# Performance work log

Measured on AMD Instinct MI355X. Metric: run time of the kernel, lower is better.

The kernel has to match this reference:

```python
import jax, jax.numpy as jnp
import numpy as np

# module hyperparameters (init kwargs)
D_MODEL = 1024
NUM_HEADS = 16
D_K = D_MODEL // NUM_HEADS
WINDOW_SIZE = 256
GLOBAL_TOKENS = 64
SEQ_LEN = 4096
BATCH = 1
NEG_INF = float('-inf')


def build_local_window_mask(seq_len, window_size, global_tokens):
    # 0 where attention is allowed, -inf where blocked
    i = jnp.arange(seq_len)[:, None]
    j = jnp.arange(seq_len)[None, :]
    allowed = (i < global_tokens) | (j < global_tokens) | (jnp.abs(i - j) <= window_size)
    return jnp.where(allowed, 0.0, NEG_INF).astype(jnp.float32)


def setup_inputs() -> dict:
    key = jax.random.key(0)
    ks = jax.random.split(key, 12)
    s = 1.0 / np.sqrt(D_MODEL)
    inp = {
        'q': jax.random.normal(ks[0], (BATCH, SEQ_LEN, D_MODEL), jnp.float32),
        'k': jax.random.normal(ks[1], (BATCH, SEQ_LEN, D_MODEL), jnp.float32),
        'v': jax.random.normal(ks[2], (BATCH, SEQ_LEN, D_MODEL), jnp.float32),
        # nn.Linear weights: shape (out, in), applied as x @ W.T + b
        'w_q': jax.random.normal(ks[3], (D_MODEL, D_MODEL), jnp.float32) * s,
        'b_q': jax.random.normal(ks[4], (D_MODEL,), jnp.float32) * s,
        'w_k': jax.random.normal(ks[5], (D_MODEL, D_MODEL), jnp.float32) * s,
        'b_k': jax.random.normal(ks[6], (D_MODEL,), jnp.float32) * s,
        'w_v': jax.random.normal(ks[7], (D_MODEL, D_MODEL), jnp.float32) * s,
        'b_v': jax.random.normal(ks[8], (D_MODEL,), jnp.float32) * s,
        'w_o': jax.random.normal(ks[9], (D_MODEL, D_MODEL), jnp.float32) * s,
        'b_o': jax.random.normal(ks[10], (D_MODEL,), jnp.float32) * s,
    }
    return inp


def reference(q, k, v, w_q, b_q, w_k, b_k, w_v, b_v, w_o, b_o):
    B, S, _ = q.shape
    scale = 1.0 / np.sqrt(D_K)

    def proj(x, w, b):  # (B,S,D) -> (B,H,S,Dk)
        y = x @ w.T + b
        return y.reshape(B, S, NUM_HEADS, D_K).transpose(0, 2, 1, 3)

    Q = proj(q, w_q, b_q)
    K = proj(k, w_k, b_k)
    V = proj(v, w_v, b_v)

    local_mask = build_local_window_mask(S, WINDOW_SIZE, GLOBAL_TOKENS)  # (S,S)
    scores = jnp.einsum('bhqd,bhkd->bhqk', Q, K) * scale + local_mask[None, None]
    attn = jax.nn.softmax(scores, axis=-1)
    out = jnp.einsum('bhqk,bhkd->bhqd', attn, V)  # (B,H,S,Dk)
    out = out.transpose(0, 2, 1, 3).reshape(B, S, D_MODEL)
    return out @ w_o.T + b_o
```

## Files before the change

kernel.cpp:

```cpp
#include <hip/hip_runtime.h>

#define S_LEN 4096
#define DMODEL 1024
#define NHEADS 16
#define DKH 64
#define WIN 256
#define GTOK 64
#define NSPLIT 8

typedef unsigned short u16t;
typedef __attribute__((ext_vector_type(8))) short short8;
typedef __attribute__((ext_vector_type(4))) float f32x4;

__device__ __forceinline__ u16t f2bf(float x) {
  union { float f; unsigned int u; } v; v.f = x;
  unsigned int r = v.u + 0x7FFFu + ((v.u >> 16) & 1u);
  return (u16t)(r >> 16);
}

__device__ __forceinline__ void gload_lds16(const u16t* g, u16t* l) {
  __builtin_amdgcn_global_load_lds(
      (const __attribute__((address_space(1))) void*)g,
      (__attribute__((address_space(3))) void*)l, 16, 0, 0);
}

__global__ void cvt4_kernel(const float* __restrict__ s0, const float* __restrict__ s1,
                            const float* __restrict__ s2, const float* __restrict__ s3,
                            u16t* __restrict__ d0, u16t* __restrict__ d1,
                            u16t* __restrict__ d2, u16t* __restrict__ d3) {
  size_t i = (size_t)blockIdx.x * 1024 + threadIdx.x * 4;
  int which = (int)(i >> 20);
  size_t local = i & ((1u << 20) - 1);
  const float* s = which == 0 ? s0 : which == 1 ? s1 : which == 2 ? s2 : s3;
  u16t* d = which == 0 ? d0 : which == 1 ? d1 : which == 2 ? d2 : d3;
  float4 f = *(const float4*)(s + local);
  unsigned int lo = (unsigned int)f2bf(f.x) | ((unsigned int)f2bf(f.y) << 16);
  unsigned int hi = (unsigned int)f2bf(f.z) | ((unsigned int)f2bf(f.w) << 16);
  *(uint2*)(d + local) = make_uint2(lo, hi);
}

__global__ void cvt3_kernel(const float* __restrict__ s0, const float* __restrict__ s1,
                            const float* __restrict__ s2,
                            u16t* __restrict__ d0, u16t* __restrict__ d1,
                            u16t* __restrict__ d2) {
  size_t i = (size_t)blockIdx.x * 1024 + threadIdx.x * 4;
  int which = (int)(i >> 22);
  size_t local = i & ((1u << 22) - 1);
  const float* s = which == 0 ? s0 : which == 1 ? s1 : s2;
  u16t* d = which == 0 ? d0 : which == 1 ? d1 : d2;
  float4 f = *(const float4*)(s + local);
  unsigned int lo = (unsigned int)f2bf(f.x) | ((unsigned int)f2bf(f.y) << 16);
  unsigned int hi = (unsigned int)f2bf(f.z) | ((unsigned int)f2bf(f.w) << 16);
  *(uint2*)(d + local) = make_uint2(lo, hi);
}

#define BN 128
#define GBK 64

template<int OUT_F32, int BMT>
__device__ __forceinline__
void gemm_body(const u16t* __restrict__ A, const u16t* __restrict__ B,
               const float* __restrict__ bias, void* __restrict__ Y,
               int N, int K, float alpha, int m0, int n0)
{
  constexpr int MF = BMT / 32;
  constexpr int CA_ISS = BMT * 2 / 64;

  __shared__ __align__(16) u16t sA[BMT * GBK];
  __shared__ __align__(16) u16t sB[BN * GBK];

  const int tid = threadIdx.x;
  const int lane = tid & 63;
  const int lr = lane & 15, lg = lane >> 4;
  const int w = tid >> 6;
  const int wm = (w >> 1) * (MF * 16), wn = (w & 1) * 64;

  f32x4 acc[MF][4] = {};
  const int nk = K / GBK;

  for (int kt = 0; kt < nk; ++kt) {
    if (kt) __syncthreads();
#pragma unroll
    for (int i = 0; i < CA_ISS; ++i) {
      int c0 = w * (BMT * 2) + i * 64;
      int c = c0 + lane;
      int row = c >> 3, g = (c & 7) ^ (row & 7);
      gload_lds16(A + (size_t)(m0 + row) * K + kt * GBK + g * 8, sA + (size_t)c0 * 8);
    }
#pragma unroll
    for (int i = 0; i < 4; ++i) {
      int c0 = w * 256 + i * 64;
      int c = c0 + lane;
      int row = c >> 3, g = (c & 7) ^ (row & 7);
      gload_lds16(B + (size_t)(n0 + row) * K + kt * GBK + g * 8, sB + (size_t)c0 * 8);
    }
    __syncthreads();

    short8 af[MF][2], bf[4][2];
#pragma unroll
    for (int mf = 0; mf < MF; ++mf)
#pragma unroll
      for (int kk = 0; kk < 2; ++kk) {
        int s = ((kk * 4 + lg) ^ (lr & 7));
        af[mf][kk] = *(const short8*)&sA[(wm + mf * 16 + lr) * GBK + s * 8];
      }
#pragma unroll
    for (int nf = 0; nf < 4; ++nf)
#pragma unroll
      for (int kk = 0; kk < 2; ++kk) {
        int s = ((kk * 4 + lg) ^ (lr & 7));
        bf[nf][kk] = *(const short8*)&sB[(wn + nf * 16 + lr) * GBK + s * 8];
      }
#pragma unroll
    for (int kk = 0; kk < 2; ++kk)
#pragma unroll
      for (int mf = 0; mf < MF; ++mf)
#pragma unroll
        for (int nf = 0; nf < 4; ++nf)
          acc[mf][nf] = __builtin_amdgcn_mfma_f32_16x16x32_bf16(af[mf][kk], bf[nf][kk], acc[mf][nf], 0, 0, 0);
  }

#pragma unroll
  for (int nf = 0; nf < 4; ++nf) {
    int col = n0 + wn + nf * 16 + lr;
    float bv = bias[col];
#pragma unroll
    for (int mf = 0; mf < MF; ++mf)
#pragma unroll
      for (int r = 0; r < 4; ++r) {
        int row = m0 + wm + mf * 16 + lg * 4 + r;
        float v = (acc[mf][nf][r] + bv) * alpha;
        if (OUT_F32) ((float*)Y)[(size_t)row * N + col] = v;
        else         ((u16t*)Y)[(size_t)row * N + col] = f2bf(v);
      }
  }
}

#define QSCALE 0.18033688011112042f
__global__ __launch_bounds__(256)
void gemm_qkv(const u16t* __restrict__ xq, const u16t* __restrict__ xk, const u16t* __restrict__ xv,
              const u16t* __restrict__ wq, const u16t* __restrict__ wk, const u16t* __restrict__ wv,
              const float* __restrict__ bq, const float* __restrict__ bk, const float* __restrict__ bv,
              u16t* __restrict__ Qp, u16t* __restrict__ Kp, u16t* __restrict__ Vp)
{
  int b = blockIdx.x;
  int wid = (b & 7) * 96 + (b >> 3);
  int z = wid >> 8;
  int rem = wid & 255;
  int my = rem >> 3, mx = rem & 7;
  const u16t* A = z == 0 ? xq : z == 1 ? xk : xv;
  const u16t* B = z == 0 ? wq : z == 1 ? wk : wv;
  const float* bi = z == 0 ? bq : z == 1 ? bk : bv;
  u16t* Y = z == 0 ? Qp : z == 1 ? Kp : Vp;
  const float alpha = (z == 0) ? QSCALE : 1.0f;
  gemm_body<0, 128>(A, B, bi, Y, DMODEL, DMODEL, alpha, my * 128, mx * BN);
}

__global__ __launch_bounds__(256)
void gemm_o(const u16t* __restrict__ A, const u16t* __restrict__ B,
            const float* __restrict__ bias, float* __restrict__ Y)
{
  int b = blockIdx.x;
  int wid = (b & 7) * 64 + (b >> 3);
  int my = wid >> 3, mx = wid & 7;
  gemm_body<1, 64>(A, B, bias, Y, DMODEL, DMODEL, 1.0f, my * 64, mx * BN);
}

#define KLDT 72

__global__ __launch_bounds__(256)
void attn_kernel(const u16t* __restrict__ Qp, const u16t* __restrict__ Kp,
                 const u16t* __restrict__ Vp, u16t* __restrict__ AO,
                 float* __restrict__ pacc, float* __restrict__ pml)
{
  __shared__ __align__(16) u16t sK[64 * KLDT];
  __shared__ __align__(16) u16t sVt[64 * KLDT];
  __shared__ __align__(16) u16t sP[4][16 * KLDT];

  const int h = blockIdx.y;
  const int tid = threadIdx.x, w = tid >> 6, lane = tid & 63;
  const int lr = lane & 15, lg = lane >> 4;

  const bool windowed = (blockIdx.x < 63);
  const int qb = windowed ? (blockIdx.x + 1) : 0;
  const int split = windowed ? 0 : (blockIdx.x - 63);
  const int qw = qb * 64 + w * 16;

  short8 qf[2];
#pragma unroll
  for (int kk = 0; kk < 2; ++kk)
    qf[kk] = *(const short8*)(Qp + (size_t)(qw + lr) * DMODEL + h * DKH + kk * 32 + lg * 8);

  f32x4 acc[4] = {};
  float m_run = -1e30f, l_run = 0.f;

  int lo = 1, nkv;
  if (windowed) {
    lo = (qb - 4 < 1) ? 1 : qb - 4;
    int hi = (qb + 4 > 63) ? 63 : qb + 4;
    nkv = hi - lo + 2;
  } else {
    nkv = 64 / NSPLIT;
  }

  uint4 rk[2], rv[2];

#define KVB(idx) (windowed ? ((idx) == 0 ? 0 : lo + (idx) - 1) : (split * (64 / NSPLIT) + (idx)))

  {
    int kv0 = KVB(0) * 64;
#pragma unroll
    for (int j = 0; j < 2; ++j) {
      int c = tid + j * 256, row = c >> 3, col8 = c & 7;
      rk[j] = *(const uint4*)(Kp + (size_t)(kv0 + row) * DMODEL + h * DKH + col8 * 8);
      rv[j] = *(const uint4*)(Vp + (size_t)(kv0 + row) * DMODEL + h * DKH + col8 * 8);
    }
#pragma unroll
    for (int j = 0; j < 2; ++j) {
      int c = tid + j * 256, row = c >> 3, col8 = c & 7;
      *(uint4*)&sK[row * KLDT + col8 * 8] = rk[j];
      union { uint4 u4; u16t s[8]; } uv; uv.u4 = rv[j];
#pragma unroll
      for (int e = 0; e < 8; ++e) {
        int d = col8 * 8 + e;
        sVt[d * KLDT + (row ^ ((d >> 3) << 3))] = uv.s[e];
      }
    }
  }
  __syncthreads();

  for (int idx = 0; idx < nkv; ++idx) {
    const int kv0 = KVB(idx) * 64;

    if (idx + 1 < nkv) {
      int nkv0 = KVB(idx + 1) * 64;
#pragma unroll
      for (int j = 0; j < 2; ++j) {
        int c = tid + j * 256, row = c >> 3, col8 = c & 7;
        rk[j] = *(const uint4*)(Kp + (size_t)(nkv0 + row) * DMODEL + h * DKH + col8 * 8);
        rv[j] = *(const uint4*)(Vp + (size_t)(nkv0 + row) * DMODEL + h * DKH + col8 * 8);
      }
    }

    f32x4 sacc[4] = {};
#pragma unroll
    for (int kk = 0; kk < 2; ++kk)
#pragma unroll
      for (int nf = 0; nf < 4; ++nf) {
        short8 kf = *(const short8*)&sK[(nf * 16 + lr) * KLDT + kk * 32 + lg * 8];
        sacc[nf] = __builtin_amdgcn_mfma_f32_16x16x32_bf16(kf, qf[kk], sacc[nf], 0, 0, 0);
      }

    if (windowed && kv0 > 0) {
      int qg = qw + lr;
#pragma unroll
      for (int nf = 0; nf < 4; ++nf)
#pragma unroll
        for (int r = 0; r < 4; ++r) {
          int sg = kv0 + nf * 16 + lg * 4 + r;
          int diff = qg - sg; if (diff < 0) diff = -diff;
          if (diff > WIN) sacc[nf][r] = -1e30f;
        }
    }

    float rm = sacc[0][0];
#pragma unroll
    for (int nf = 0; nf < 4; ++nf)
#pragma unroll
      for (int r = 0; r < 4; ++r)
        rm = fmaxf(rm, sacc[nf][r]);
    rm = fmaxf(rm, __shfl_xor(rm, 16));
    rm = fmaxf(rm, __shfl_xor(rm, 32));
    float mnew = fmaxf(m_run, rm);
    float corr = exp2f(m_run - mnew);
    m_run = mnew;

    float p[4][4];
    float rs = 0.f;
#pragma unroll
    for (int nf = 0; nf < 4; ++nf)
#pragma unroll
      for (int r = 0; r < 4; ++r) {
        float e = exp2f(sacc[nf][r] - mnew);
        p[nf][r] = e;
        rs += e;
      }
    rs += __shfl_xor(rs, 16);
    rs += __shfl_xor(rs, 32);
    l_run = l_run * corr + rs;

    float cq[4];
#pragma unroll
    for (int r = 0; r < 4; ++r) cq[r] = __shfl(corr, lg * 4 + r);
#pragma unroll
    for (int nf = 0; nf < 4; ++nf)
#pragma unroll
      for (int r = 0; r < 4; ++r) acc[nf][r] *= cq[r];

#pragma unroll
    for (int nf = 0; nf < 4; ++nf) {
      uint2 w2;
      w2.x = (unsigned int)f2bf(p[nf][0]) | ((unsigned int)f2bf(p[nf][1]) << 16);
      w2.y = (unsigned int)f2bf(p[nf][2]) | ((unsigned int)f2bf(p[nf][3]) << 16);
      *(uint2*)&sP[w][lr * KLDT + nf * 16 + lg * 4] = w2;
    }

#pragma unroll
    for (int kk = 0; kk < 2; ++kk) {
      short8 pf = *(const short8*)&sP[w][lr * KLDT + kk * 32 + lg * 8];
#pragma unroll
      for (int nf = 0; nf < 4; ++nf) {
        int d = nf * 16 + lr;
        int s0 = kk * 32 + lg * 8;
        short8 vf = *(const short8*)&sVt[d * KLDT + (s0 ^ ((d >> 3) << 3))];
        acc[nf] = __builtin_amdgcn_mfma_f32_16x16x32_bf16(pf, vf, acc[nf], 0, 0, 0);
      }
    }

    if (idx + 1 < nkv) {
      __syncthreads();
#pragma unroll
      for (int j = 0; j < 2; ++j) {
        int c = tid + j * 256, row = c >> 3, col8 = c & 7;
        *(uint4*)&sK[row * KLDT + col8 * 8] = rk[j];
        union { uint4 u4; u16t s[8]; } uv; uv.u4 = rv[j];
#pragma unroll
        for (int e = 0; e < 8; ++e) {
          int d = col8 * 8 + e;
          sVt[d * KLDT + (row ^ ((d >> 3) << 3))] = uv.s[e];
        }
      }
      __syncthreads();
    }
  }
#undef KVB

  if (windowed) {
    float lq[4];
#pragma unroll
    for (int r = 0; r < 4; ++r) lq[r] = __shfl(l_run, lg * 4 + r);
#pragma unroll
    for (int nf = 0; nf < 4; ++nf)
#pragma unroll
      for (int r = 0; r < 4; ++r) {
        float v = acc[nf][r] / lq[r];
        AO[(size_t)(qw + lg * 4 + r) * DMODEL + h * DKH + nf * 16 + lr] = f2bf(v);
      }
  } else {
    const int pbase = (h * NSPLIT + split) * 64;
#pragma unroll
    for (int nf = 0; nf < 4; ++nf)
#pragma unroll
      for (int r = 0; r < 4; ++r)
        pacc[(size_t)(pbase + w * 16 + lg * 4 + r) * 64 + nf * 16 + lr] = acc[nf][r];
    if (lane < 16) {
      int b = (pbase + w * 16 + lane) * 2;
      pml[b] = m_run;
      pml[b + 1] = l_run;
    }
  }
}

__global__ __launch_bounds__(256)
void merge_kernel(const float* __restrict__ pacc, const float* __restrict__ pml,
                  u16t* __restrict__ AO)
{
  const int h = blockIdx.x;
  const int tid = threadIdx.x;
  const int row = tid >> 2;
  const int d0 = (tid & 3) * 16;

  float M = -1e30f;
#pragma unroll
  for (int s = 0; s < NSPLIT; ++s)
    M = fmaxf(M, pml[((h * NSPLIT + s) * 64 + row) * 2]);

  float L = 0.f;
  float o[16];
#pragma unroll
  for (int e = 0; e < 16; ++e) o[e] = 0.f;

#pragma unroll
  for (int s = 0; s < NSPLIT; ++s) {
    int b = ((h * NSPLIT + s) * 64 + row) * 2;
    float sc = exp2f(pml[b] - M);
    L += pml[b + 1] * sc;
    const float4* a = (const float4*)(pacc + ((size_t)(h * NSPLIT + s) * 64 + row) * 64 + d0);
#pragma unroll
    for (int q4 = 0; q4 < 4; ++q4) {
      float4 av = a[q4];
      o[q4 * 4 + 0] += av.x * sc;
      o[q4 * 4 + 1] += av.y * sc;
      o[q4 * 4 + 2] += av.z * sc;
      o[q4 * 4 + 3] += av.w * sc;
    }
  }
  float inv = 1.f / L;
#pragma unroll
  for (int e = 0; e < 16; ++e)
    AO[(size_t)row * DMODEL + h * DKH + d0 + e] = f2bf(o[e] * inv);
}

extern "C" void kernel_launch(void* const* d_in, const int* in_sizes, int n_in,
                              void* d_out, int out_size, void* d_ws, size_t ws_size,
                              hipStream_t stream) {
  const float* q   = (const float*)d_in[0];
  const float* k   = (const float*)d_in[1];
  const float* v   = (const float*)d_in[2];
  const float* w_q = (const float*)d_in[3];
  const float* b_q = (const float*)d_in[4];
  const float* w_k = (const float*)d_in[5];
  const float* b_k = (const float*)d_in[6];
  const float* w_v = (const float*)d_in[7];
  const float* b_v = (const float*)d_in[8];
  const float* w_o = (const float*)d_in[9];
  const float* b_o = (const float*)d_in[10];

  u16t* ws = (u16t*)d_ws;
  const size_t SZX = (size_t)S_LEN * DMODEL;
  const size_t SZW = (size_t)DMODEL * DMODEL;
  u16t* xq  = ws;
  u16t* xk  = xq + SZX;
  u16t* xv  = xk + SZX;
  u16t* wb0 = xv + SZX;
  u16t* wb1 = wb0 + SZW;
  u16t* wb2 = wb1 + SZW;
  u16t* wb3 = wb2 + SZW;
  u16t* Qp  = wb3 + SZW;
  u16t* Kp  = Qp + SZX;
  u16t* Vp  = Kp + SZX;
  u16t* AO  = xk;
  float* pacc = (float*)xq;
  float* pml  = pacc + (size_t)NHEADS * NSPLIT * 64 * 64;

  dim3 blk(256);

  cvt4_kernel<<<(int)(4 * SZW / 1024), blk, 0, stream>>>(w_q, w_k, w_v, w_o, wb0, wb1, wb2, wb3);
  cvt3_kernel<<<(int)(3 * SZX / 1024), blk, 0, stream>>>(q, k, v, xq, xk, xv);

  gemm_qkv<<<768, blk, 0, stream>>>(xq, xk, xv, wb0, wb1, wb2, b_q, b_k, b_v, Qp, Kp, Vp);

  attn_kernel<<<dim3(63 + NSPLIT, NHEADS), blk, 0, stream>>>(Qp, Kp, Vp, AO, pacc, pml);
  merge_kernel<<<NHEADS, blk, 0, stream>>>(pacc, pml, AO);

  gemm_o<<<512, blk, 0, stream>>>(AO, wb3, b_o, (float*)d_out);
}
```

Measured before the change: 129.6 us.

## Produce V transposed in QKV GEMM and double-buffer attention K/V via direct LDS loads

The V projection is now computed as W_v·X^T, so V is written already transposed (bias applied per row). This lets the attention kernel stage K and V^T tiles straight into swizzled, double-buffered LDS with global_load_lds, replacing the register staging and scalar transpose scatter. That removes one barrier per KV tile and most of the LDS write work. The kernel also applies the window mask only on the edge blocks and skips the online-softmax rescale unless the running max grows by more than a threshold. These changes add LDS footprint and rely on the lazy-rescale bound to keep the exponentials from overflowing.

```diff
diff --git a/kernel.cpp b/kernel.cpp
--- a/kernel.cpp
+++ b/kernel.cpp
@@ -57,7 +57,7 @@
 #define BN 128
 #define GBK 64
 
-template<int OUT_F32, int BMT>
+template<int OUT_F32, int BMT, int BIAS_ROW>
 __device__ __forceinline__
 void gemm_body(const u16t* __restrict__ A, const u16t* __restrict__ B,
                const float* __restrict__ bias, void* __restrict__ Y,
@@ -123,12 +123,13 @@
 #pragma unroll
   for (int nf = 0; nf < 4; ++nf) {
     int col = n0 + wn + nf * 16 + lr;
-    float bv = bias[col];
+    float bvc = BIAS_ROW ? 0.f : bias[col];
 #pragma unroll
     for (int mf = 0; mf < MF; ++mf)
 #pragma unroll
       for (int r = 0; r < 4; ++r) {
         int row = m0 + wm + mf * 16 + lg * 4 + r;
+        float bv = BIAS_ROW ? bias[row] : bvc;
         float v = (acc[mf][nf][r] + bv) * alpha;
         if (OUT_F32) ((float*)Y)[(size_t)row * N + col] = v;
         else         ((u16t*)Y)[(size_t)row * N + col] = f2bf(v);
@@ -141,19 +142,19 @@
 void gemm_qkv(const u16t* __restrict__ xq, const u16t* __restrict__ xk, const u16t* __restrict__ xv,
               const u16t* __restrict__ wq, const u16t* __restrict__ wk, const u16t* __restrict__ wv,
               const float* __restrict__ bq, const float* __restrict__ bk, const float* __restrict__ bv,
-              u16t* __restrict__ Qp, u16t* __restrict__ Kp, u16t* __restrict__ Vp)
+              u16t* __restrict__ Qp, u16t* __restrict__ Kp, u16t* __restrict__ Vt)
 {
   int b = blockIdx.x;
   int wid = (b & 7) * 96 + (b >> 3);
   int z = wid >> 8;
   int rem = wid & 255;
-  int my = rem >> 3, mx = rem & 7;
-  const u16t* A = z == 0 ? xq : z == 1 ? xk : xv;
-  const u16t* B = z == 0 ? wq : z == 1 ? wk : wv;
-  const float* bi = z == 0 ? bq : z == 1 ? bk : bv;
-  u16t* Y = z == 0 ? Qp : z == 1 ? Kp : Vp;
-  const float alpha = (z == 0) ? QSCALE : 1.0f;
-  gemm_body<0, 128>(A, B, bi, Y, DMODEL, DMODEL, alpha, my * 128, mx * BN);
+  if (z == 0) {
+    gemm_body<0, 128, 0>(xq, wq, bq, Qp, DMODEL, DMODEL, QSCALE, (rem >> 3) * 128, (rem & 7) * BN);
+  } else if (z == 1) {
+    gemm_body<0, 128, 0>(xk, wk, bk, Kp, DMODEL, DMODEL, 1.0f, (rem >> 3) * 128, (rem & 7) * BN);
+  } else {
+    gemm_body<0, 128, 1>(wv, xv, bv, Vt, S_LEN, DMODEL, 1.0f, (rem & 7) * 128, (rem >> 3) * BN);
+  }
 }
 
 __global__ __launch_bounds__(256)
@@ -163,18 +164,18 @@
   int b = blockIdx.x;
   int wid = (b & 7) * 64 + (b >> 3);
   int my = wid >> 3, mx = wid & 7;
-  gemm_body<1, 64>(A, B, bias, Y, DMODEL, DMODEL, 1.0f, my * 64, mx * BN);
+  gemm_body<1, 64, 0>(A, B, bias, Y, DMODEL, DMODEL, 1.0f, my * 64, mx * BN);
 }
 
 #define KLDT 72
 
 __global__ __launch_bounds__(256)
 void attn_kernel(const u16t* __restrict__ Qp, const u16t* __restrict__ Kp,
-                 const u16t* __restrict__ Vp, u16t* __restrict__ AO,
+                 const u16t* __restrict__ Vt, u16t* __restrict__ AO,
                  float* __restrict__ pacc, float* __restrict__ pml)
 {
-  __shared__ __align__(16) u16t sK[64 * KLDT];
-  __shared__ __align__(16) u16t sVt[64 * KLDT];
+  __shared__ __align__(16) u16t sK[2][64 * 64];
+  __shared__ __align__(16) u16t sV[2][64 * 64];
   __shared__ __align__(16) u16t sP[4][16 * KLDT];
 
   const int h = blockIdx.y;
@@ -203,55 +204,45 @@
     nkv = 64 / NSPLIT;
   }
 
-  uint4 rk[2], rv[2];
-
 #define KVB(idx) (windowed ? ((idx) == 0 ? 0 : lo + (idx) - 1) : (split * (64 / NSPLIT) + (idx)))
 
-  {
-    int kv0 = KVB(0) * 64;
+  auto stage = [&](int buf, int kvb) {
+    int kv0 = kvb * 64;
 #pragma unroll
     for (int j = 0; j < 2; ++j) {
-      int c = tid + j * 256, row = c >> 3, col8 = c & 7;
-      rk[j] = *(const uint4*)(Kp + (size_t)(kv0 + row) * DMODEL + h * DKH + col8 * 8);
-      rv[j] = *(const uint4*)(Vp + (size_t)(kv0 + row) * DMODEL + h * DKH + col8 * 8);
+      int c = tid + j * 256;
+      int row = c >> 3, g = (c & 7) ^ (row & 7);
+      gload_lds16(Kp + (size_t)(kv0 + row) * DMODEL + h * DKH + g * 8, &sK[buf][c * 8]);
     }
 #pragma unroll
     for (int j = 0; j < 2; ++j) {
-      int c = tid + j * 256, row = c >> 3, col8 = c & 7;
-      *(uint4*)&sK[row * KLDT + col8 * 8] = rk[j];
-      union { uint4 u4; u16t s[8]; } uv; uv.u4 = rv[j];
-#pragma unroll
-      for (int e = 0; e < 8; ++e) {
-        int d = col8 * 8 + e;
-        sVt[d * KLDT + (row ^ ((d >> 3) << 3))] = uv.s[e];
-      }
-    }
-  }
+      int c = tid + j * 256;
+      int row = c >> 3, g = (c & 7) ^ (row & 7);
+      gload_lds16(Vt + (size_t)(h * DKH + row) * S_LEN + kv0 + g * 8, &sV[buf][c * 8]);
+    }
+  };
+
+  stage(0, KVB(0));
   __syncthreads();
 
   for (int idx = 0; idx < nkv; ++idx) {
-    const int kv0 = KVB(idx) * 64;
-
-    if (idx + 1 < nkv) {
-      int nkv0 = KVB(idx + 1) * 64;
-#pragma unroll
-      for (int j = 0; j < 2; ++j) {
-        int c = tid + j * 256, row = c >> 3, col8 = c & 7;
-        rk[j] = *(const uint4*)(Kp + (size_t)(nkv0 + row) * DMODEL + h * DKH + col8 * 8);
-        rv[j] = *(const uint4*)(Vp + (size_t)(nkv0 + row) * DMODEL + h * DKH + col8 * 8);
-      }
-    }
+    const int buf = idx & 1;
+    const int kvb = KVB(idx);
+    const int kv0 = kvb * 64;
+
+    if (idx + 1 < nkv) stage(buf ^ 1, KVB(idx + 1));
 
     f32x4 sacc[4] = {};
 #pragma unroll
     for (int kk = 0; kk < 2; ++kk)
 #pragma unroll
       for (int nf = 0; nf < 4; ++nf) {
-        short8 kf = *(const short8*)&sK[(nf * 16 + lr) * KLDT + kk * 32 + lg * 8];
+        int s = ((kk * 4 + lg) ^ (lr & 7));
+        short8 kf = *(const short8*)&sK[buf][(nf * 16 + lr) * 64 + s * 8];
         sacc[nf] = __builtin_amdgcn_mfma_f32_16x16x32_bf16(kf, qf[kk], sacc[nf], 0, 0, 0);
       }
 
-    if (windowed && kv0 > 0) {
+    if (windowed && (kvb == qb + 4 || (kvb == qb - 4 && kvb > 0))) {
       int qg = qw + lr;
 #pragma unroll
       for (int nf = 0; nf < 4; ++nf)
@@ -271,9 +262,20 @@
         rm = fmaxf(rm, sacc[nf][r]);
     rm = fmaxf(rm, __shfl_xor(rm, 16));
     rm = fmaxf(rm, __shfl_xor(rm, 32));
-    float mnew = fmaxf(m_run, rm);
-    float corr = exp2f(m_run - mnew);
-    m_run = mnew;
+
+    if (!__all(rm <= m_run + 11.0f)) {
+      float mnew = fmaxf(m_run, rm);
+      float corr = exp2f(m_run - mnew);
+      m_run = mnew;
+      l_run *= corr;
+      float cq[4];
+#pragma unroll
+      for (int r = 0; r < 4; ++r) cq[r] = __shfl(corr, lg * 4 + r);
+#pragma unroll
+      for (int nf = 0; nf < 4; ++nf)
+#pragma unroll
+        for (int r = 0; r < 4; ++r) acc[nf][r] *= cq[r];
+    }
 
     float p[4][4];
     float rs = 0.f;
@@ -281,21 +283,13 @@
     for (int nf = 0; nf < 4; ++nf)
 #pragma unroll
       for (int r = 0; r < 4; ++r) {
-        float e = exp2f(sacc[nf][r] - mnew);
+        float e = exp2f(sacc[nf][r] - m_run);
         p[nf][r] = e;
         rs += e;
       }
     rs += __shfl_xor(rs, 16);
     rs += __shfl_xor(rs, 32);
-    l_run = l_run * corr + rs;
-
-    float cq[4];
-#pragma unroll
-    for (int r = 0; r < 4; ++r) cq[r] = __shfl(corr, lg * 4 + r);
-#pragma unroll
-    for (int nf = 0; nf < 4; ++nf)
-#pragma unroll
-      for (int r = 0; r < 4; ++r) acc[nf][r] *= cq[r];
+    l_run += rs;
 
 #pragma unroll
     for (int nf = 0; nf < 4; ++nf) {
@@ -310,28 +304,13 @@
       short8 pf = *(const short8*)&sP[w][lr * KLDT + kk * 32 + lg * 8];
 #pragma unroll
       for (int nf = 0; nf < 4; ++nf) {
-        int d = nf * 16 + lr;
-        int s0 = kk * 32 + lg * 8;
-        short8 vf = *(const short8*)&sVt[d * KLDT + (s0 ^ ((d >> 3) << 3))];
+        int s = ((kk * 4 + lg) ^ (lr & 7));
+        short8 vf = *(const short8*)&sV[buf][(nf * 16 + lr) * 64 + s * 8];
         acc[nf] = __builtin_amdgcn_mfma_f32_16x16x32_bf16(pf, vf, acc[nf], 0, 0, 0);
       }
     }
 
-    if (idx + 1 < nkv) {
-      __syncthreads();
-#pragma unroll
-      for (int j = 0; j < 2; ++j) {
-        int c = tid + j * 256, row = c >> 3, col8 = c & 7;
-        *(uint4*)&sK[row * KLDT + col8 * 8] = rk[j];
-        union { uint4 u4; u16t s[8]; } uv; uv.u4 = rv[j];
-#pragma unroll
-        for (int e = 0; e < 8; ++e) {
-          int d = col8 * 8 + e;
-          sVt[d * KLDT + (row ^ ((d >> 3) << 3))] = uv.s[e];
-        }
-      }
-      __syncthreads();
-    }
+    if (idx + 1 < nkv) __syncthreads();
   }
 #undef KVB
 
@@ -428,7 +407,7 @@
   u16t* wb3 = wb2 + SZW;
   u16t* Qp  = wb3 + SZW;
   u16t* Kp  = Qp + SZX;
-  u16t* Vp  = Kp + SZX;
+  u16t* Vt  = Kp + SZX;
   u16t* AO  = xk;
   float* pacc = (float*)xq;
   float* pml  = pacc + (size_t)NHEADS * NSPLIT * 64 * 64;
@@ -438,9 +417,9 @@
   cvt4_kernel<<<(int)(4 * SZW / 1024), blk, 0, stream>>>(w_q, w_k, w_v, w_o, wb0, wb1, wb2, wb3);
   cvt3_kernel<<<(int)(3 * SZX / 1024), blk, 0, stream>>>(q, k, v, xq, xk, xv);
 
-  gemm_qkv<<<768, blk, 0, stream>>>(xq, xk, xv, wb0, wb1, wb2, b_q, b_k, b_v, Qp, Kp, Vp);
-
-  attn_kernel<<<dim3(63 + NSPLIT, NHEADS), blk, 0, stream>>>(Qp, Kp, Vp, AO, pacc, pml);
+  gemm_qkv<<<768, blk, 0, stream>>>(xq, xk, xv, wb0, wb1, wb2, b_q, b_k, b_v, Qp, Kp, Vt);
+
+  attn_kernel<<<dim3(63 + NSPLIT, NHEADS), blk, 0, stream>>>(Qp, Kp, Vt, AO, pacc, pml);
   merge_kernel<<<NHEADS, blk, 0, stream>>>(pacc, pml, AO);
 
   gemm_o<<<512, blk, 0, stream>>>(AO, wb3, b_o, (float*)d_out);
```

Result: faster. 122.2 us (-5.8%).
